# Kernel tuning notes

Hardware: AMD Instinct MI355X
Metric: run time of the kernel (lower is better)

Reference implementation:

```python
import jax, jax.numpy as jnp
import numpy as np

D_MODEL, D_HIDDEN, N_EXPERTS, TOP_K = 1024, 2048, 8, 2


def setup_inputs() -> dict:
    key = jax.random.key(0)
    ks = jax.random.split(key, 8)
    s_in = 1.0 / np.sqrt(D_MODEL)
    s_hid = 1.0 / np.sqrt(D_HIDDEN)
    return {
        "x": jax.random.normal(ks[0], (1, 2048, D_MODEL), dtype=jnp.float32),
        # stacked expert weights, stored (in, out) so y = x @ W + b
        "W1": jax.random.normal(ks[1], (N_EXPERTS, D_MODEL, D_HIDDEN), dtype=jnp.float32) * s_in,
        "b1": jnp.zeros((N_EXPERTS, D_HIDDEN), dtype=jnp.float32),
        "W2": jax.random.normal(ks[2], (N_EXPERTS, D_MODEL, D_HIDDEN), dtype=jnp.float32) * s_in,
        "b2": jnp.zeros((N_EXPERTS, D_HIDDEN), dtype=jnp.float32),
        "Wo": jax.random.normal(ks[3], (N_EXPERTS, D_HIDDEN, D_MODEL), dtype=jnp.float32) * s_hid,
        "bo": jnp.zeros((N_EXPERTS, D_MODEL), dtype=jnp.float32),
        "Wr": jax.random.normal(ks[4], (D_MODEL, N_EXPERTS), dtype=jnp.float32) * s_in,
        "br": jnp.zeros((N_EXPERTS,), dtype=jnp.float32),
    }


def reference(x, W1, b1, W2, b2, Wo, bo, Wr, br):
    B, S, D = x.shape
    T = B * S
    xf = x.reshape(T, D)

    # router
    logits = xf @ Wr + br                      # [T, E]
    probs = jax.nn.softmax(logits, axis=-1)
    topk_probs, topk_idx = jax.lax.top_k(probs, TOP_K)  # [T, K]

    # combine weights: c[t, e] = sum_k topk_probs[t, k] * 1[topk_idx[t, k] == e]
    c = jnp.zeros((T, N_EXPERTS), dtype=xf.dtype)
    c = c.at[jnp.arange(T)[:, None], topk_idx].add(topk_probs)  # [T, E]

    # per-expert SwiGLU FFN applied densely, then masked-combined (same math
    # as the original gather/scatter loop since c[t,e]=0 for unrouted experts)
    h = jnp.einsum('td,edh->eth', xf, W1) + b1[:, None, :]   # [E, T, H]
    g = jnp.einsum('td,edh->eth', xf, W2) + b2[:, None, :]
    y = jnp.einsum('eth,ehd->etd', h * jax.nn.silu(g), Wo) + bo[:, None, :]
    out = jnp.einsum('etd,te->td', y, c).reshape(B, S, D)

    probs_mean = probs.mean(axis=0)
    lb_loss = (probs_mean * probs_mean).sum() * N_EXPERTS
    return out, lb_loss
```

## Files before the change

kernel.cpp:

```cpp
#include <hip/hip_runtime.h>
#include <hip/hip_bf16.h>

#define T_TOK 2048
#define DM 1024
#define DH 2048
#define NE 8

using bf16x8 = __attribute__((ext_vector_type(8))) short;
using f32x4  = __attribute__((ext_vector_type(4))) float;

__device__ __forceinline__ unsigned short f2bf(float f) {
  union { float f; unsigned u; } v; v.f = f;
  unsigned r = v.u + 0x7FFFu + ((v.u >> 16) & 1u);
  return (unsigned short)(r >> 16);
}
__device__ __forceinline__ unsigned pk2(float a, float b) {
  return (unsigned)f2bf(a) | ((unsigned)f2bf(b) << 16);
}

#define GLOAD16(gsrc, ldst)                                                        \
  __builtin_amdgcn_global_load_lds(                                                \
      (const __attribute__((address_space(1))) unsigned int*)(gsrc),               \
      (__attribute__((address_space(3))) unsigned int*)(ldst), 16, 0, 0)

__global__ void k_init(int* __restrict__ cnt) {
  if (threadIdx.x < NE) cnt[threadIdx.x] = 0;
}

__global__ __launch_bounds__(256) void k_router(
    const float* __restrict__ x, const float* __restrict__ Wr, const float* __restrict__ br,
    int* __restrict__ cnt, int* __restrict__ idx, float* __restrict__ wgt,
    int* __restrict__ t2r, float* __restrict__ probs, unsigned short* __restrict__ xb)
{
  const int wave = threadIdx.x >> 6, l = threadIdx.x & 63;
  const int t = blockIdx.x * 4 + wave;
  float xv[16];
#pragma unroll
  for (int i = 0; i < 16; ++i) xv[i] = x[t*DM + l + 64*i];
#pragma unroll
  for (int i = 0; i < 16; ++i) xb[t*DM + l + 64*i] = f2bf(xv[i]);

  float acc[8] = {0.f,0.f,0.f,0.f,0.f,0.f,0.f,0.f};
#pragma unroll
  for (int i = 0; i < 16; ++i) {
    const float4* wp = (const float4*)&Wr[(size_t)(l + 64*i)*NE];
    float4 wa = wp[0], wb = wp[1];
    acc[0] += xv[i]*wa.x; acc[1] += xv[i]*wa.y; acc[2] += xv[i]*wa.z; acc[3] += xv[i]*wa.w;
    acc[4] += xv[i]*wb.x; acc[5] += xv[i]*wb.y; acc[6] += xv[i]*wb.z; acc[7] += xv[i]*wb.w;
  }
#pragma unroll
  for (int e = 0; e < 8; ++e) {
#pragma unroll
    for (int off = 32; off; off >>= 1) acc[e] += __shfl_xor(acc[e], off, 64);
    acc[e] += br[e];
  }
  float mx = acc[0];
#pragma unroll
  for (int e = 1; e < 8; ++e) mx = fmaxf(mx, acc[e]);
  float p[8], s = 0.f;
#pragma unroll
  for (int e = 0; e < 8; ++e) { p[e] = expf(acc[e] - mx); s += p[e]; }
  float inv = 1.f / s;
#pragma unroll
  for (int e = 0; e < 8; ++e) p[e] *= inv;

  int e0 = 0; float p0 = p[0];
#pragma unroll
  for (int e = 1; e < 8; ++e) if (p[e] > p0) { p0 = p[e]; e0 = e; }
  int e1 = -1; float p1 = -1.f;
#pragma unroll
  for (int e = 0; e < 8; ++e) { if (e == e0) continue; if (p[e] > p1) { p1 = p[e]; e1 = e; } }

  if (l == 0) {
#pragma unroll
    for (int e = 0; e < 8; ++e) probs[t*NE + e] = p[e];
    int pos0 = atomicAdd(&cnt[e0], 1);
    idx[e0*T_TOK + pos0] = t; wgt[e0*T_TOK + pos0] = p0;
    t2r[t*2 + 0] = e0*T_TOK + pos0;
    int pos1 = atomicAdd(&cnt[e1], 1);
    idx[e1*T_TOK + pos1] = t; wgt[e1*T_TOK + pos1] = p1;
    t2r[t*2 + 1] = e1*T_TOK + pos1;
  }
}

__global__ __launch_bounds__(256) void k_finalize(
    const int* __restrict__ cnt, int* __restrict__ rb,
    const float* __restrict__ probs, float* __restrict__ out)
{
  __shared__ float red[8][256];
  const int tid = threadIdx.x;
  float s[8] = {0.f,0.f,0.f,0.f,0.f,0.f,0.f,0.f};
  for (int t = tid; t < T_TOK; t += 256) {
#pragma unroll
    for (int e = 0; e < 8; ++e) s[e] += probs[t*NE + e];
  }
#pragma unroll
  for (int e = 0; e < 8; ++e) red[e][tid] = s[e];
  __syncthreads();
  for (int w = 128; w > 0; w >>= 1) {
    if (tid < w) {
#pragma unroll
      for (int e = 0; e < 8; ++e) red[e][tid] += red[e][tid + w];
    }
    __syncthreads();
  }
  if (tid == 0) {
    float lb = 0.f;
#pragma unroll
    for (int e = 0; e < 8; ++e) {
      float mean = red[e][0] * (1.f / T_TOK);
      lb += mean * mean;
    }
    out[2097152] = lb * NE;
    int r = 0;
#pragma unroll
    for (int e = 0; e < 8; ++e) { rb[e] = r; r += cnt[e]; }
  }
}

__global__ __launch_bounds__(256) void k_convAll(
    const float* __restrict__ W1, const float* __restrict__ W2, const float* __restrict__ Wo,
    unsigned short* __restrict__ W1T, unsigned short* __restrict__ W2T,
    unsigned short* __restrict__ WoT)
{
  int b = blockIdx.x;
  const float* in; unsigned short* outT; int R, C;
  if (b < 4096)      { in = W1; outT = W1T; R = DM; C = DH; }
  else if (b < 8192) { in = W2; outT = W2T; R = DM; C = DH; b -= 4096; }
  else               { in = Wo; outT = WoT; R = DH; C = DM; b -= 8192; }
  const int nC = C / 64;
  const int tilesPerE = (R / 64) * nC;
  const int e  = b / tilesPerE;
  const int tb = b % tilesPerE;
  const int r0 = (tb / nC) * 64, c0 = (tb % nC) * 64;

  __shared__ float t[64][65];
  const int tid = threadIdx.x;
  const int lr = tid >> 4, lc = (tid & 15) * 4;
#pragma unroll
  for (int i = 0; i < 4; ++i) {
    float4 v = *(const float4*)&in[((size_t)e*R + r0 + lr + i*16)*C + c0 + lc];
    t[lr + i*16][lc+0] = v.x; t[lr + i*16][lc+1] = v.y;
    t[lr + i*16][lc+2] = v.z; t[lr + i*16][lc+3] = v.w;
  }
  __syncthreads();
  const int oc = tid >> 3;
  const int od = (tid & 7) * 8;
#pragma unroll
  for (int i = 0; i < 2; ++i) {
    int c = oc + i*32;
    uint4 v;
    v.x = pk2(t[od+0][c], t[od+1][c]);
    v.y = pk2(t[od+2][c], t[od+3][c]);
    v.z = pk2(t[od+4][c], t[od+5][c]);
    v.w = pk2(t[od+6][c], t[od+7][c]);
    *(uint4*)&outT[((size_t)e*C + c0 + c)*R + r0 + od] = v;
  }
}

#define TM1 128
#define TN1 64
#define BKK 64

__global__ __launch_bounds__(256) void k_ffn1b(
    const unsigned short* __restrict__ xb,
    const unsigned short* __restrict__ W1T, const float* __restrict__ b1,
    const unsigned short* __restrict__ W2T, const float* __restrict__ b2,
    const int* __restrict__ cnt, const int* __restrict__ rbp,
    const int* __restrict__ idx, unsigned short* __restrict__ act)
{
  const int e = blockIdx.z, mt = blockIdx.y, nt = blockIdx.x;
  const int Me = cnt[e];
  const int m0 = mt * TM1;
  if (m0 >= Me) return;
  const int n0 = nt * TN1;

  __shared__ __align__(16) unsigned short As[2][TM1*BKK];
  __shared__ __align__(16) unsigned short Bh[2][TN1*BKK];
  __shared__ __align__(16) unsigned short Bg[2][TN1*BKK];
  __shared__ int toks[TM1];

  const int tid = threadIdx.x;
  if (tid < TM1) toks[tid] = idx[e*T_TOK + min(m0 + tid, Me - 1)];
  __syncthreads();

  const int lane = tid & 63;
  const int wave = tid >> 6;
  const int wm = wave >> 1, wn = wave & 1;
  const int row16 = lane & 15, kg = lane >> 4;
  const int sl = lane & 7;
  const int lr = lane >> 3;

  const unsigned short* asrc[4];
#pragma unroll
  for (int i = 0; i < 4; ++i) {
    int r = (wave*4 + i)*8 + lr;
    asrc[i] = &xb[(size_t)toks[r]*DM + ((sl ^ (r & 7)) * 8)];
  }
  const unsigned short *bsrc1[2], *bsrc2[2];
#pragma unroll
  for (int j = 0; j < 2; ++j) {
    int r = (wave*2 + j)*8 + lr;
    size_t gb = ((size_t)e*DH + n0 + r)*DM + ((sl ^ (r & 7)) * 8);
    bsrc1[j] = &W1T[gb]; bsrc2[j] = &W2T[gb];
  }

#define STAGE1(buf, k0)                                                   \
  do {                                                                    \
    _Pragma("unroll")                                                     \
    for (int i = 0; i < 4; ++i)                                           \
      GLOAD16(asrc[i] + (k0), &As[buf][(wave*4 + i)*512]);                \
    _Pragma("unroll")                                                     \
    for (int j = 0; j < 2; ++j) {                                         \
      GLOAD16(bsrc1[j] + (k0), &Bh[buf][(wave*2 + j)*512]);               \
      GLOAD16(bsrc2[j] + (k0), &Bg[buf][(wave*2 + j)*512]);               \
    }                                                                     \
  } while (0)

  f32x4 ah[4][2], ag[4][2];
#pragma unroll
  for (int i = 0; i < 4; ++i)
#pragma unroll
    for (int j = 0; j < 2; ++j) { ah[i][j] = 0.f; ag[i][j] = 0.f; }

  STAGE1(0, 0);
  __syncthreads();

  for (int kt = 0; kt < DM/BKK; ++kt) {
    const int cur = kt & 1;
    if (kt + 1 < DM/BKK) STAGE1(cur ^ 1, (kt + 1) * BKK);
#pragma unroll
    for (int ks = 0; ks < 2; ++ks) {
      const int kslot = ks*4 + kg;
      bf16x8 a[4], vbh[2], vbg[2];
#pragma unroll
      for (int mi = 0; mi < 4; ++mi) {
        int m = wm*64 + mi*16 + row16;
        a[mi] = *(const bf16x8*)&As[cur][m*BKK + ((kslot ^ (m & 7)) * 8)];
      }
#pragma unroll
      for (int ni = 0; ni < 2; ++ni) {
        int n = wn*32 + ni*16 + row16;
        int off = n*BKK + ((kslot ^ (n & 7)) * 8);
        vbh[ni] = *(const bf16x8*)&Bh[cur][off];
        vbg[ni] = *(const bf16x8*)&Bg[cur][off];
      }
#pragma unroll
      for (int mi = 0; mi < 4; ++mi)
#pragma unroll
        for (int ni = 0; ni < 2; ++ni) {
          ah[mi][ni] = __builtin_amdgcn_mfma_f32_16x16x32_bf16(a[mi], vbh[ni], ah[mi][ni], 0, 0, 0);
          ag[mi][ni] = __builtin_amdgcn_mfma_f32_16x16x32_bf16(a[mi], vbg[ni], ag[mi][ni], 0, 0, 0);
        }
    }
    __syncthreads();
  }

  const int rb = rbp[e];
#pragma unroll
  for (int mi = 0; mi < 4; ++mi) {
#pragma unroll
    for (int i = 0; i < 4; ++i) {
      int rloc = wm*64 + mi*16 + (lane >> 4)*4 + i;
      int m = m0 + rloc;
      if (m < Me) {
#pragma unroll
        for (int ni = 0; ni < 2; ++ni) {
          int col = n0 + wn*32 + ni*16 + row16;
          float h = ah[mi][ni][i] + b1[e*DH + col];
          float g = ag[mi][ni][i] + b2[e*DH + col];
          float sg = g / (1.f + __expf(-g));
          act[(size_t)(rb + m)*DH + col] = f2bf(h * sg);
        }
      }
    }
  }
#undef STAGE1
}

__global__ __launch_bounds__(256) void k_ffn2b(
    const unsigned short* __restrict__ act,
    const unsigned short* __restrict__ WoT, const float* __restrict__ bo,
    const int* __restrict__ cnt, const int* __restrict__ rbp,
    float* __restrict__ ys)
{
  const int e = blockIdx.z, mt = blockIdx.y, nt = blockIdx.x;
  const int Me = cnt[e];
  const int m0 = mt * TM1;
  if (m0 >= Me) return;
  const int n0 = nt * TN1;
  const int rb = rbp[e];

  __shared__ __align__(16) unsigned short As[2][TM1*BKK];
  __shared__ __align__(16) unsigned short Bs[2][TN1*BKK];

  const int tid = threadIdx.x;
  const int lane = tid & 63;
  const int wave = tid >> 6;
  const int wm = wave >> 1, wn = wave & 1;
  const int row16 = lane & 15, kg = lane >> 4;
  const int sl = lane & 7;
  const int lr = lane >> 3;

  const unsigned short* asrc[4];
#pragma unroll
  for (int i = 0; i < 4; ++i) {
    int r = (wave*4 + i)*8 + lr;
    int grow = rb + min(m0 + r, Me - 1);
    asrc[i] = &act[(size_t)grow*DH + ((sl ^ (r & 7)) * 8)];
  }
  const unsigned short* bsrc[2];
#pragma unroll
  for (int j = 0; j < 2; ++j) {
    int r = (wave*2 + j)*8 + lr;
    bsrc[j] = &WoT[((size_t)e*DM + n0 + r)*DH + ((sl ^ (r & 7)) * 8)];
  }

#define STAGE2(buf, k0)                                                   \
  do {                                                                    \
    _Pragma("unroll")                                                     \
    for (int i = 0; i < 4; ++i)                                           \
      GLOAD16(asrc[i] + (k0), &As[buf][(wave*4 + i)*512]);                \
    _Pragma("unroll")                                                     \
    for (int j = 0; j < 2; ++j)                                           \
      GLOAD16(bsrc[j] + (k0), &Bs[buf][(wave*2 + j)*512]);                \
  } while (0)

  f32x4 acc[4][2];
#pragma unroll
  for (int i = 0; i < 4; ++i)
#pragma unroll
    for (int j = 0; j < 2; ++j) acc[i][j] = 0.f;

  STAGE2(0, 0);
  __syncthreads();

  for (int kt = 0; kt < DH/BKK; ++kt) {
    const int cur = kt & 1;
    if (kt + 1 < DH/BKK) STAGE2(cur ^ 1, (kt + 1) * BKK);
#pragma unroll
    for (int ks = 0; ks < 2; ++ks) {
      const int kslot = ks*4 + kg;
      bf16x8 a[4], b[2];
#pragma unroll
      for (int mi = 0; mi < 4; ++mi) {
        int m = wm*64 + mi*16 + row16;
        a[mi] = *(const bf16x8*)&As[cur][m*BKK + ((kslot ^ (m & 7)) * 8)];
      }
#pragma unroll
      for (int ni = 0; ni < 2; ++ni) {
        int n = wn*32 + ni*16 + row16;
        b[ni] = *(const bf16x8*)&Bs[cur][n*BKK + ((kslot ^ (n & 7)) * 8)];
      }
#pragma unroll
      for (int mi = 0; mi < 4; ++mi)
#pragma unroll
        for (int ni = 0; ni < 2; ++ni)
          acc[mi][ni] = __builtin_amdgcn_mfma_f32_16x16x32_bf16(a[mi], b[ni], acc[mi][ni], 0, 0, 0);
    }
    __syncthreads();
  }

#pragma unroll
  for (int mi = 0; mi < 4; ++mi) {
#pragma unroll
    for (int i = 0; i < 4; ++i) {
      int rloc = wm*64 + mi*16 + (lane >> 4)*4 + i;
      int m = m0 + rloc;
      if (m < Me) {
#pragma unroll
        for (int ni = 0; ni < 2; ++ni) {
          int col = n0 + wn*32 + ni*16 + row16;
          ys[(size_t)(rb + m)*DM + col] = acc[mi][ni][i] + bo[e*DM + col];
        }
      }
    }
  }
#undef STAGE2
}

__global__ __launch_bounds__(256) void k_combine(
    const float* __restrict__ ys, const int* __restrict__ t2r,
    const int* __restrict__ rbp, const float* __restrict__ wgt,
    float* __restrict__ out)
{
  const int t = blockIdx.x, tid = threadIdx.x;
  const int c0 = t2r[t*2 + 0], c1 = t2r[t*2 + 1];
  const float w0 = wgt[c0], w1 = wgt[c1];
  const int r0 = rbp[c0 >> 11] + (c0 & 2047);
  const int r1 = rbp[c1 >> 11] + (c1 & 2047);
  const float4* p0 = (const float4*)&ys[(size_t)r0*DM];
  const float4* p1 = (const float4*)&ys[(size_t)r1*DM];
  float4* po = (float4*)&out[(size_t)t*DM];
  float4 a = p0[tid], b = p1[tid];
  float4 r;
  r.x = w0*a.x + w1*b.x; r.y = w0*a.y + w1*b.y;
  r.z = w0*a.z + w1*b.z; r.w = w0*a.w + w1*b.w;
  po[tid] = r;
}

extern "C" void kernel_launch(void* const* d_in, const int* in_sizes, int n_in,
                              void* d_out, int out_size, void* d_ws, size_t ws_size,
                              hipStream_t stream)
{
  const float* x  = (const float*)d_in[0];
  const float* W1 = (const float*)d_in[1];
  const float* b1 = (const float*)d_in[2];
  const float* W2 = (const float*)d_in[3];
  const float* b2 = (const float*)d_in[4];
  const float* Wo = (const float*)d_in[5];
  const float* bo = (const float*)d_in[6];
  const float* Wr = (const float*)d_in[7];
  const float* br = (const float*)d_in[8];
  float* out = (float*)d_out;

  char* ws = (char*)d_ws;
  int*   cnt   = (int*)(ws + 0);
  int*   rb    = (int*)(ws + 256);
  int*   t2r   = (int*)(ws + 512);
  int*   idx   = (int*)(ws + 32*1024);
  float* wgt   = (float*)(ws + 96*1024);
  float* probs = (float*)(ws + 160*1024);
  unsigned short* xb  = (unsigned short*)(ws + 256*1024);
  unsigned short* act = (unsigned short*)(ws + 5ull*1024*1024);
  float* ysb = (float*)(ws + 21ull*1024*1024);
  unsigned short* W1T = (unsigned short*)(ws + 40ull*1024*1024);
  unsigned short* W2T = (unsigned short*)(ws + 72ull*1024*1024);
  unsigned short* WoT = (unsigned short*)(ws + 104ull*1024*1024);

  k_init<<<1, 64, 0, stream>>>(cnt);
  k_router<<<T_TOK/4, 256, 0, stream>>>(x, Wr, br, cnt, idx, wgt, t2r, probs, xb);
  k_finalize<<<1, 256, 0, stream>>>(cnt, rb, probs, out);
  k_convAll<<<12288, 256, 0, stream>>>(W1, W2, Wo, W1T, W2T, WoT);
  k_ffn1b<<<dim3(DH/TN1, T_TOK/TM1, NE), 256, 0, stream>>>(xb, W1T, b1, W2T, b2, cnt, rb, idx, act);
  k_ffn2b<<<dim3(DM/TN1, T_TOK/TM1, NE), 256, 0, stream>>>(act, WoT, bo, cnt, rb, ysb);
  k_combine<<<T_TOK, 256, 0, stream>>>(ysb, t2r, rb, wgt, out);
}
```

Before: 225.9 us.

## Compact expert m-tile grid, fuse router with weight conversion, drop double buffering

Merges the router and the weight transpose/convert kernels into one launch, so one fewer kernel runs and the two jobs share the machine. The finalize kernel builds a compact table of (expert, m-tile) pairs, and the FFN grids index that table instead of launching a sparse 3D grid where most blocks exit early. The LDS double buffering in both GEMMs is removed, halving shared memory per block for more occupancy, at the cost of no load/compute overlap within a block. MT_MAX of 40 is enough because the eight experts together hold at most 36 tiles of 128 rows.

```diff
diff --git a/kernel.cpp b/kernel.cpp
--- a/kernel.cpp
+++ b/kernel.cpp
@@ -5,6 +5,7 @@
 #define DM 1024
 #define DH 2048
 #define NE 8
+#define MT_MAX 40
 
 using bf16x8 = __attribute__((ext_vector_type(8))) short;
 using f32x4  = __attribute__((ext_vector_type(4))) float;
@@ -27,103 +28,69 @@
   if (threadIdx.x < NE) cnt[threadIdx.x] = 0;
 }
 
-__global__ __launch_bounds__(256) void k_router(
+__global__ __launch_bounds__(256) void k_rconv(
     const float* __restrict__ x, const float* __restrict__ Wr, const float* __restrict__ br,
     int* __restrict__ cnt, int* __restrict__ idx, float* __restrict__ wgt,
-    int* __restrict__ t2r, float* __restrict__ probs, unsigned short* __restrict__ xb)
-{
-  const int wave = threadIdx.x >> 6, l = threadIdx.x & 63;
-  const int t = blockIdx.x * 4 + wave;
-  float xv[16];
-#pragma unroll
-  for (int i = 0; i < 16; ++i) xv[i] = x[t*DM + l + 64*i];
-#pragma unroll
-  for (int i = 0; i < 16; ++i) xb[t*DM + l + 64*i] = f2bf(xv[i]);
-
-  float acc[8] = {0.f,0.f,0.f,0.f,0.f,0.f,0.f,0.f};
-#pragma unroll
-  for (int i = 0; i < 16; ++i) {
-    const float4* wp = (const float4*)&Wr[(size_t)(l + 64*i)*NE];
-    float4 wa = wp[0], wb = wp[1];
-    acc[0] += xv[i]*wa.x; acc[1] += xv[i]*wa.y; acc[2] += xv[i]*wa.z; acc[3] += xv[i]*wa.w;
-    acc[4] += xv[i]*wb.x; acc[5] += xv[i]*wb.y; acc[6] += xv[i]*wb.z; acc[7] += xv[i]*wb.w;
-  }
-#pragma unroll
-  for (int e = 0; e < 8; ++e) {
-#pragma unroll
-    for (int off = 32; off; off >>= 1) acc[e] += __shfl_xor(acc[e], off, 64);
-    acc[e] += br[e];
-  }
-  float mx = acc[0];
-#pragma unroll
-  for (int e = 1; e < 8; ++e) mx = fmaxf(mx, acc[e]);
-  float p[8], s = 0.f;
-#pragma unroll
-  for (int e = 0; e < 8; ++e) { p[e] = expf(acc[e] - mx); s += p[e]; }
-  float inv = 1.f / s;
-#pragma unroll
-  for (int e = 0; e < 8; ++e) p[e] *= inv;
-
-  int e0 = 0; float p0 = p[0];
-#pragma unroll
-  for (int e = 1; e < 8; ++e) if (p[e] > p0) { p0 = p[e]; e0 = e; }
-  int e1 = -1; float p1 = -1.f;
-#pragma unroll
-  for (int e = 0; e < 8; ++e) { if (e == e0) continue; if (p[e] > p1) { p1 = p[e]; e1 = e; } }
-
-  if (l == 0) {
-#pragma unroll
-    for (int e = 0; e < 8; ++e) probs[t*NE + e] = p[e];
-    int pos0 = atomicAdd(&cnt[e0], 1);
-    idx[e0*T_TOK + pos0] = t; wgt[e0*T_TOK + pos0] = p0;
-    t2r[t*2 + 0] = e0*T_TOK + pos0;
-    int pos1 = atomicAdd(&cnt[e1], 1);
-    idx[e1*T_TOK + pos1] = t; wgt[e1*T_TOK + pos1] = p1;
-    t2r[t*2 + 1] = e1*T_TOK + pos1;
-  }
-}
-
-__global__ __launch_bounds__(256) void k_finalize(
-    const int* __restrict__ cnt, int* __restrict__ rb,
-    const float* __restrict__ probs, float* __restrict__ out)
-{
-  __shared__ float red[8][256];
-  const int tid = threadIdx.x;
-  float s[8] = {0.f,0.f,0.f,0.f,0.f,0.f,0.f,0.f};
-  for (int t = tid; t < T_TOK; t += 256) {
-#pragma unroll
-    for (int e = 0; e < 8; ++e) s[e] += probs[t*NE + e];
-  }
-#pragma unroll
-  for (int e = 0; e < 8; ++e) red[e][tid] = s[e];
-  __syncthreads();
-  for (int w = 128; w > 0; w >>= 1) {
-    if (tid < w) {
-#pragma unroll
-      for (int e = 0; e < 8; ++e) red[e][tid] += red[e][tid + w];
-    }
-    __syncthreads();
-  }
-  if (tid == 0) {
-    float lb = 0.f;
-#pragma unroll
-    for (int e = 0; e < 8; ++e) {
-      float mean = red[e][0] * (1.f / T_TOK);
-      lb += mean * mean;
-    }
-    out[2097152] = lb * NE;
-    int r = 0;
-#pragma unroll
-    for (int e = 0; e < 8; ++e) { rb[e] = r; r += cnt[e]; }
-  }
-}
-
-__global__ __launch_bounds__(256) void k_convAll(
+    int* __restrict__ t2r, float* __restrict__ probs, unsigned short* __restrict__ xb,
     const float* __restrict__ W1, const float* __restrict__ W2, const float* __restrict__ Wo,
     unsigned short* __restrict__ W1T, unsigned short* __restrict__ W2T,
     unsigned short* __restrict__ WoT)
 {
-  int b = blockIdx.x;
+  __shared__ float t[64][65];
+  if (blockIdx.x < 512) {
+    const int wave = threadIdx.x >> 6, l = threadIdx.x & 63;
+    const int tok = blockIdx.x * 4 + wave;
+    float xv[16];
+#pragma unroll
+    for (int i = 0; i < 16; ++i) xv[i] = x[tok*DM + l + 64*i];
+#pragma unroll
+    for (int i = 0; i < 16; ++i) xb[tok*DM + l + 64*i] = f2bf(xv[i]);
+
+    float acc[8] = {0.f,0.f,0.f,0.f,0.f,0.f,0.f,0.f};
+#pragma unroll
+    for (int i = 0; i < 16; ++i) {
+      const float4* wp = (const float4*)&Wr[(size_t)(l + 64*i)*NE];
+      float4 wa = wp[0], wb = wp[1];
+      acc[0] += xv[i]*wa.x; acc[1] += xv[i]*wa.y; acc[2] += xv[i]*wa.z; acc[3] += xv[i]*wa.w;
+      acc[4] += xv[i]*wb.x; acc[5] += xv[i]*wb.y; acc[6] += xv[i]*wb.z; acc[7] += xv[i]*wb.w;
+    }
+#pragma unroll
+    for (int e = 0; e < 8; ++e) {
+#pragma unroll
+      for (int off = 32; off; off >>= 1) acc[e] += __shfl_xor(acc[e], off, 64);
+      acc[e] += br[e];
+    }
+    float mx = acc[0];
+#pragma unroll
+    for (int e = 1; e < 8; ++e) mx = fmaxf(mx, acc[e]);
+    float p[8], s = 0.f;
+#pragma unroll
+    for (int e = 0; e < 8; ++e) { p[e] = expf(acc[e] - mx); s += p[e]; }
+    float inv = 1.f / s;
+#pragma unroll
+    for (int e = 0; e < 8; ++e) p[e] *= inv;
+
+    int e0 = 0; float p0 = p[0];
+#pragma unroll
+    for (int e = 1; e < 8; ++e) if (p[e] > p0) { p0 = p[e]; e0 = e; }
+    int e1 = -1; float p1 = -1.f;
+#pragma unroll
+    for (int e = 0; e < 8; ++e) { if (e == e0) continue; if (p[e] > p1) { p1 = p[e]; e1 = e; } }
+
+    if (l == 0) {
+#pragma unroll
+      for (int e = 0; e < 8; ++e) probs[tok*NE + e] = p[e];
+      int pos0 = atomicAdd(&cnt[e0], 1);
+      idx[e0*T_TOK + pos0] = tok; wgt[e0*T_TOK + pos0] = p0;
+      t2r[tok*2 + 0] = e0*T_TOK + pos0;
+      int pos1 = atomicAdd(&cnt[e1], 1);
+      idx[e1*T_TOK + pos1] = tok; wgt[e1*T_TOK + pos1] = p1;
+      t2r[tok*2 + 1] = e1*T_TOK + pos1;
+    }
+    return;
+  }
+
+  int b = blockIdx.x - 512;
   const float* in; unsigned short* outT; int R, C;
   if (b < 4096)      { in = W1; outT = W1T; R = DM; C = DH; }
   else if (b < 8192) { in = W2; outT = W2T; R = DM; C = DH; b -= 4096; }
@@ -134,7 +101,6 @@
   const int tb = b % tilesPerE;
   const int r0 = (tb / nC) * 64, c0 = (tb % nC) * 64;
 
-  __shared__ float t[64][65];
   const int tid = threadIdx.x;
   const int lr = tid >> 4, lc = (tid & 15) * 4;
 #pragma unroll
@@ -158,6 +124,47 @@
   }
 }
 
+__global__ __launch_bounds__(256) void k_finalize(
+    const int* __restrict__ cnt, int* __restrict__ rb,
+    const float* __restrict__ probs, float* __restrict__ out,
+    int* __restrict__ MTp, int* __restrict__ mtab)
+{
+  __shared__ float red[8][256];
+  const int tid = threadIdx.x;
+  float s[8] = {0.f,0.f,0.f,0.f,0.f,0.f,0.f,0.f};
+  for (int t = tid; t < T_TOK; t += 256) {
+#pragma unroll
+    for (int e = 0; e < 8; ++e) s[e] += probs[t*NE + e];
+  }
+#pragma unroll
+  for (int e = 0; e < 8; ++e) red[e][tid] = s[e];
+  __syncthreads();
+  for (int w = 128; w > 0; w >>= 1) {
+    if (tid < w) {
+#pragma unroll
+      for (int e = 0; e < 8; ++e) red[e][tid] += red[e][tid + w];
+    }
+    __syncthreads();
+  }
+  if (tid == 0) {
+    float lb = 0.f;
+#pragma unroll
+    for (int e = 0; e < 8; ++e) {
+      float mean = red[e][0] * (1.f / T_TOK);
+      lb += mean * mean;
+    }
+    out[2097152] = lb * NE;
+    int r = 0, mc = 0;
+#pragma unroll
+    for (int e = 0; e < 8; ++e) {
+      rb[e] = r; r += cnt[e];
+      int nmt = (cnt[e] + 127) / 128;
+      for (int j = 0; j < nmt; ++j) mtab[mc++] = (e << 16) | j;
+    }
+    *MTp = mc;
+  }
+}
+
 #define TM1 128
 #define TN1 64
 #define BKK 64
@@ -167,17 +174,21 @@
     const unsigned short* __restrict__ W1T, const float* __restrict__ b1,
     const unsigned short* __restrict__ W2T, const float* __restrict__ b2,
     const int* __restrict__ cnt, const int* __restrict__ rbp,
-    const int* __restrict__ idx, unsigned short* __restrict__ act)
-{
-  const int e = blockIdx.z, mt = blockIdx.y, nt = blockIdx.x;
+    const int* __restrict__ idx, unsigned short* __restrict__ act,
+    const int* __restrict__ MTp, const int* __restrict__ mtab)
+{
+  const int mtg = blockIdx.y;
+  if (mtg >= *MTp) return;
+  const int code = mtab[mtg];
+  const int e = code >> 16, mt = code & 0xffff;
   const int Me = cnt[e];
   const int m0 = mt * TM1;
-  if (m0 >= Me) return;
+  const int nt = blockIdx.x;
   const int n0 = nt * TN1;
 
-  __shared__ __align__(16) unsigned short As[2][TM1*BKK];
-  __shared__ __align__(16) unsigned short Bh[2][TN1*BKK];
-  __shared__ __align__(16) unsigned short Bg[2][TN1*BKK];
+  __shared__ __align__(16) unsigned short As[TM1*BKK];
+  __shared__ __align__(16) unsigned short Bh[TN1*BKK];
+  __shared__ __align__(16) unsigned short Bg[TN1*BKK];
   __shared__ int toks[TM1];
 
   const int tid = threadIdx.x;
@@ -205,30 +216,22 @@
     bsrc1[j] = &W1T[gb]; bsrc2[j] = &W2T[gb];
   }
 
-#define STAGE1(buf, k0)                                                   \
-  do {                                                                    \
-    _Pragma("unroll")                                                     \
-    for (int i = 0; i < 4; ++i)                                           \
-      GLOAD16(asrc[i] + (k0), &As[buf][(wave*4 + i)*512]);                \
-    _Pragma("unroll")                                                     \
-    for (int j = 0; j < 2; ++j) {                                         \
-      GLOAD16(bsrc1[j] + (k0), &Bh[buf][(wave*2 + j)*512]);               \
-      GLOAD16(bsrc2[j] + (k0), &Bg[buf][(wave*2 + j)*512]);               \
-    }                                                                     \
-  } while (0)
-
   f32x4 ah[4][2], ag[4][2];
 #pragma unroll
   for (int i = 0; i < 4; ++i)
 #pragma unroll
     for (int j = 0; j < 2; ++j) { ah[i][j] = 0.f; ag[i][j] = 0.f; }
 
-  STAGE1(0, 0);
-  __syncthreads();
-
-  for (int kt = 0; kt < DM/BKK; ++kt) {
-    const int cur = kt & 1;
-    if (kt + 1 < DM/BKK) STAGE1(cur ^ 1, (kt + 1) * BKK);
+  for (int k0 = 0; k0 < DM; k0 += BKK) {
+#pragma unroll
+    for (int i = 0; i < 4; ++i)
+      GLOAD16(asrc[i] + k0, &As[(wave*4 + i)*512]);
+#pragma unroll
+    for (int j = 0; j < 2; ++j) {
+      GLOAD16(bsrc1[j] + k0, &Bh[(wave*2 + j)*512]);
+      GLOAD16(bsrc2[j] + k0, &Bg[(wave*2 + j)*512]);
+    }
+    __syncthreads();
 #pragma unroll
     for (int ks = 0; ks < 2; ++ks) {
       const int kslot = ks*4 + kg;
@@ -236,14 +239,14 @@
 #pragma unroll
       for (int mi = 0; mi < 4; ++mi) {
         int m = wm*64 + mi*16 + row16;
-        a[mi] = *(const bf16x8*)&As[cur][m*BKK + ((kslot ^ (m & 7)) * 8)];
+        a[mi] = *(const bf16x8*)&As[m*BKK + ((kslot ^ (m & 7)) * 8)];
       }
 #pragma unroll
       for (int ni = 0; ni < 2; ++ni) {
         int n = wn*32 + ni*16 + row16;
         int off = n*BKK + ((kslot ^ (n & 7)) * 8);
-        vbh[ni] = *(const bf16x8*)&Bh[cur][off];
-        vbg[ni] = *(const bf16x8*)&Bg[cur][off];
+        vbh[ni] = *(const bf16x8*)&Bh[off];
+        vbg[ni] = *(const bf16x8*)&Bg[off];
       }
 #pragma unroll
       for (int mi = 0; mi < 4; ++mi)
@@ -275,24 +278,27 @@
       }
     }
   }
-#undef STAGE1
 }
 
 __global__ __launch_bounds__(256) void k_ffn2b(
     const unsigned short* __restrict__ act,
     const unsigned short* __restrict__ WoT, const float* __restrict__ bo,
     const int* __restrict__ cnt, const int* __restrict__ rbp,
-    float* __restrict__ ys)
-{
-  const int e = blockIdx.z, mt = blockIdx.y, nt = blockIdx.x;
+    float* __restrict__ ys,
+    const int* __restrict__ MTp, const int* __restrict__ mtab)
+{
+  const int mtg = blockIdx.y;
+  if (mtg >= *MTp) return;
+  const int code = mtab[mtg];
+  const int e = code >> 16, mt = code & 0xffff;
   const int Me = cnt[e];
   const int m0 = mt * TM1;
-  if (m0 >= Me) return;
+  const int nt = blockIdx.x;
   const int n0 = nt * TN1;
   const int rb = rbp[e];
 
-  __shared__ __align__(16) unsigned short As[2][TM1*BKK];
-  __shared__ __align__(16) unsigned short Bs[2][TN1*BKK];
+  __shared__ __align__(16) unsigned short As[TM1*BKK];
+  __shared__ __align__(16) unsigned short Bs[TN1*BKK];
 
   const int tid = threadIdx.x;
   const int lane = tid & 63;
@@ -316,28 +322,20 @@
     bsrc[j] = &WoT[((size_t)e*DM + n0 + r)*DH + ((sl ^ (r & 7)) * 8)];
   }
 
-#define STAGE2(buf, k0)                                                   \
-  do {                                                                    \
-    _Pragma("unroll")                                                     \
-    for (int i = 0; i < 4; ++i)                                           \
-      GLOAD16(asrc[i] + (k0), &As[buf][(wave*4 + i)*512]);                \
-    _Pragma("unroll")                                                     \
-    for (int j = 0; j < 2; ++j)                                           \
-      GLOAD16(bsrc[j] + (k0), &Bs[buf][(wave*2 + j)*512]);                \
-  } while (0)
-
   f32x4 acc[4][2];
 #pragma unroll
   for (int i = 0; i < 4; ++i)
 #pragma unroll
     for (int j = 0; j < 2; ++j) acc[i][j] = 0.f;
 
-  STAGE2(0, 0);
-  __syncthreads();
-
-  for (int kt = 0; kt < DH/BKK; ++kt) {
-    const int cur = kt & 1;
-    if (kt + 1 < DH/BKK) STAGE2(cur ^ 1, (kt + 1) * BKK);
+  for (int k0 = 0; k0 < DH; k0 += BKK) {
+#pragma unroll
+    for (int i = 0; i < 4; ++i)
+      GLOAD16(asrc[i] + k0, &As[(wave*4 + i)*512]);
+#pragma unroll
+    for (int j = 0; j < 2; ++j)
+      GLOAD16(bsrc[j] + k0, &Bs[(wave*2 + j)*512]);
+    __syncthreads();
 #pragma unroll
     for (int ks = 0; ks < 2; ++ks) {
       const int kslot = ks*4 + kg;
@@ -345,12 +343,12 @@
 #pragma unroll
       for (int mi = 0; mi < 4; ++mi) {
         int m = wm*64 + mi*16 + row16;
-        a[mi] = *(const bf16x8*)&As[cur][m*BKK + ((kslot ^ (m & 7)) * 8)];
+        a[mi] = *(const bf16x8*)&As[m*BKK + ((kslot ^ (m & 7)) * 8)];
       }
 #pragma unroll
       for (int ni = 0; ni < 2; ++ni) {
         int n = wn*32 + ni*16 + row16;
-        b[ni] = *(const bf16x8*)&Bs[cur][n*BKK + ((kslot ^ (n & 7)) * 8)];
+        b[ni] = *(const bf16x8*)&Bs[n*BKK + ((kslot ^ (n & 7)) * 8)];
       }
 #pragma unroll
       for (int mi = 0; mi < 4; ++mi)
@@ -376,7 +374,6 @@
       }
     }
   }
-#undef STAGE2
 }
 
 __global__ __launch_bounds__(256) void k_combine(
@@ -416,8 +413,10 @@
 
   char* ws = (char*)d_ws;
   int*   cnt   = (int*)(ws + 0);
-  int*   rb    = (int*)(ws + 256);
-  int*   t2r   = (int*)(ws + 512);
+  int*   rb    = (int*)(ws + 64);
+  int*   MTp   = (int*)(ws + 128);
+  int*   mtab  = (int*)(ws + 192);
+  int*   t2r   = (int*)(ws + 4096);
   int*   idx   = (int*)(ws + 32*1024);
   float* wgt   = (float*)(ws + 96*1024);
   float* probs = (float*)(ws + 160*1024);
@@ -429,10 +428,10 @@
   unsigned short* WoT = (unsigned short*)(ws + 104ull*1024*1024);
 
   k_init<<<1, 64, 0, stream>>>(cnt);
-  k_router<<<T_TOK/4, 256, 0, stream>>>(x, Wr, br, cnt, idx, wgt, t2r, probs, xb);
-  k_finalize<<<1, 256, 0, stream>>>(cnt, rb, probs, out);
-  k_convAll<<<12288, 256, 0, stream>>>(W1, W2, Wo, W1T, W2T, WoT);
-  k_ffn1b<<<dim3(DH/TN1, T_TOK/TM1, NE), 256, 0, stream>>>(xb, W1T, b1, W2T, b2, cnt, rb, idx, act);
-  k_ffn2b<<<dim3(DM/TN1, T_TOK/TM1, NE), 256, 0, stream>>>(act, WoT, bo, cnt, rb, ysb);
+  k_rconv<<<512 + 12288, 256, 0, stream>>>(x, Wr, br, cnt, idx, wgt, t2r, probs, xb,
+                                           W1, W2, Wo, W1T, W2T, WoT);
+  k_finalize<<<1, 256, 0, stream>>>(cnt, rb, probs, out, MTp, mtab);
+  k_ffn1b<<<dim3(DH/TN1, MT_MAX), 256, 0, stream>>>(xb, W1T, b1, W2T, b2, cnt, rb, idx, act, MTp, mtab);
+  k_ffn2b<<<dim3(DM/TN1, MT_MAX), 256, 0, stream>>>(act, WoT, bo, cnt, rb, ysb, MTp, mtab);
   k_combine<<<T_TOK, 256, 0, stream>>>(ysb, t2r, rb, wgt, out);
 }
```

Result: faster. 213.9 us (-5.3%).
